# Kernel tuning notes

Measured on AMD Instinct MI355X. Metric: run time of the kernel, lower is better.

The kernel has to match this reference:

```python
import jax, jax.numpy as jnp
import numpy as np

LN_EPS = 1e-5
BN_EPS = 1e-5
ATTN_EPS = 1e-6

def _ln(x, g, b):
    m = x.mean(-1, keepdims=True)
    v = x.var(-1, keepdims=True)
    return (x - m) / jnp.sqrt(v + LN_EPS) * g + b

def setup_inputs() -> dict:
    key = jax.random.key(0)
    ks = jax.random.split(key, 16)
    B, C, N = 4, 256, 8192
    s = 0.05
    def rn(k, shape, scale=1.0):
        return jax.random.normal(k, shape, jnp.float32) * scale
    return {
        "x1": rn(ks[0], (B, C, N)),
        "x2": rn(ks[1], (B, C, N)),
        "Wq": rn(ks[2], (C, C), s), "bq": rn(ks[3], (C,), s),
        "Wk": rn(ks[4], (C, C), s), "bk": rn(ks[5], (C,), s),
        "Wv": rn(ks[6], (C, C), s), "bv": rn(ks[7], (C,), s),
        "threshold": jnp.array([0.1], jnp.float32),
        "W1": rn(ks[8], (2 * C, 2 * C), s),
        "W2": rn(ks[9], (C, 2 * C), s),
        "g1": jnp.ones((C,), jnp.float32), "b1": jnp.zeros((C,), jnp.float32),
        "g2": jnp.ones((C,), jnp.float32), "b2": jnp.zeros((C,), jnp.float32),
        "Wa": rn(ks[10], (C, C), s), "ba": rn(ks[11], (C,), s),
        "bn_g": jnp.ones((C,), jnp.float32), "bn_b": jnp.zeros((C,), jnp.float32),
        "bn_m": jnp.zeros((C,), jnp.float32), "bn_v": jnp.ones((C,), jnp.float32),
    }

def reference(x1, x2, Wq, bq, Wk, bk, Wv, bv, threshold, W1, W2,
              g1, b1, g2, b2, Wa, ba, bn_g, bn_b, bn_m, bn_v):
    B, C, N = x1.shape
    H = 4
    d = C // H
    def conv1x1(x, W, b):  # nn.Conv1d(C, C, 1): [B,C,N] -> [B,C,N]
        return jnp.einsum('bcn,oc->bon', x, W) + b[:, None]
    # projections -> [B, N, H, d]
    q = conv1x1(x1, Wq, bq).transpose(0, 2, 1).reshape(B, N, H, d)
    k = conv1x1(x2, Wk, bk).transpose(0, 2, 1).reshape(B, N, H, d)
    v = conv1x1(x2, Wv, bv).transpose(0, 2, 1).reshape(B, N, H, d)
    # DynamicSparseLinearAttention
    Q = jax.nn.elu(q) + 1.0
    K = jax.nn.elu(k) + 1.0
    S = v.shape[1]
    vals = v / S
    KV = jnp.einsum('nshd,nshv->nhdv', K, vals)               # [B,H,d,d]
    scores = jnp.einsum('nlhd,nhd->nlh', Q, K.sum(axis=1))    # [B,N,H]
    sparse = jnp.where(scores > threshold[0], scores, 0.0)
    Z = 1.0 / (sparse + ATTN_EPS)
    msg = jnp.einsum('nlhd,nhdv,nlh->nlhv', Q, KV, Z) * S     # [B,N,H,d]
    # view [B,N,C]; the transpose(1,2).transpose(1,2) in torch cancels
    msg = msg.reshape(B, N, H * d)
    msg = _ln(msg, g1, b1)
    msg = jnp.concatenate([x1.transpose(0, 2, 1), msg], axis=2)  # [B,N,2C]
    msg = jax.nn.relu(msg @ W1.T) @ W2.T                         # [B,N,C]
    msg = _ln(msg, g2, b2).transpose(0, 2, 1)                    # [B,C,N]
    # aug shortcut: conv1x1 + BatchNorm1d (eval mode, running stats)
    aug = conv1x1(x1, Wa, ba)
    aug = (aug - bn_m[None, :, None]) / jnp.sqrt(bn_v[None, :, None] + BN_EPS)
    aug = aug * bn_g[None, :, None] + bn_b[None, :, None]
    return msg + x1 + aug
```

## Files before the change

### kernel.cpp

```cpp
#include <hip/hip_runtime.h>

#define BB 4
#define CC 256
#define NN 8192
#define HH 4
#define NCH 16

typedef unsigned short u16;
typedef __bf16 bf16x8 __attribute__((ext_vector_type(8)));
typedef float f32x4 __attribute__((ext_vector_type(4)));

__device__ __forceinline__ float bf2f(unsigned u) {
  return __uint_as_float(u << 16);
}
__device__ __forceinline__ u16 f2bf(float f) {
  unsigned u = __float_as_uint(f);
  return (u16)((u + 0x7fffu + ((u >> 16) & 1u)) >> 16);
}
__device__ __forceinline__ void bf8_to_f32(uint4 r, float* f) {
  f[0] = __uint_as_float(r.x << 16); f[1] = __uint_as_float(r.x & 0xffff0000u);
  f[2] = __uint_as_float(r.y << 16); f[3] = __uint_as_float(r.y & 0xffff0000u);
  f[4] = __uint_as_float(r.z << 16); f[5] = __uint_as_float(r.z & 0xffff0000u);
  f[6] = __uint_as_float(r.w << 16); f[7] = __uint_as_float(r.w & 0xffff0000u);
}
__device__ __forceinline__ void bf4_to_f32(uint2 r, float* f) {
  f[0] = __uint_as_float(r.x << 16); f[1] = __uint_as_float(r.x & 0xffff0000u);
  f[2] = __uint_as_float(r.y << 16); f[3] = __uint_as_float(r.y & 0xffff0000u);
}
__device__ __forceinline__ void gload16(const u16* g, u16* l) {
  __builtin_amdgcn_global_load_lds(
      (const __attribute__((address_space(1))) unsigned int*)g,
      (__attribute__((address_space(3))) unsigned int*)l, 16, 0, 0);
}

__global__ __launch_bounds__(256) void cvt_all_kernel(
    const float* __restrict__ wq, const float* __restrict__ wk,
    const float* __restrict__ wv, const float* __restrict__ wa,
    const float* __restrict__ w1, const float* __restrict__ w2,
    u16* __restrict__ oq, u16* __restrict__ ok, u16* __restrict__ ov,
    u16* __restrict__ oa, u16* __restrict__ o1, u16* __restrict__ o2) {
  int i = blockIdx.x * 256 + threadIdx.x;
  const float* src;
  u16* dst;
  int off;
  if (i < 65536) { src = wq; dst = oq; off = i; }
  else if (i < 131072) { src = wk; dst = ok; off = i - 65536; }
  else if (i < 196608) { src = wv; dst = ov; off = i - 131072; }
  else if (i < 262144) { src = wa; dst = oa; off = i - 196608; }
  else if (i < 524288) { src = w1; dst = o1; off = i - 262144; }
  else { src = w2; dst = o2; off = i - 524288; }
  dst[off] = f2bf(src[off]);
}

__global__ __launch_bounds__(256) void transpose_kernel(const float* __restrict__ x1,
                                                        const float* __restrict__ x2,
                                                        u16* __restrict__ x1t,
                                                        u16* __restrict__ x2t) {
  __shared__ float T[64][65];
  const int bz = blockIdx.z;
  const int b = bz & 3;
  const float* x = (bz < 4) ? x1 : x2;
  u16* xt = (bz < 4) ? x1t : x2t;
  const int c0 = blockIdx.y * 64, n0 = blockIdx.x * 64;
  const float* xp = x + ((size_t)b * CC + c0) * NN + n0;
#pragma unroll
  for (int it = 0; it < 4; ++it) {
    int idx = threadIdx.x + it * 256;
    int r = idx >> 4, seg = idx & 15;
    float4 v = *(const float4*)(xp + (size_t)r * NN + seg * 4);
    T[r][seg * 4 + 0] = v.x; T[r][seg * 4 + 1] = v.y;
    T[r][seg * 4 + 2] = v.z; T[r][seg * 4 + 3] = v.w;
  }
  __syncthreads();
  u16* op = xt + ((size_t)b * NN + n0) * CC + c0;
  const int j = threadIdx.x >> 2, g = threadIdx.x & 3;
#pragma unroll
  for (int i = 0; i < 4; ++i) {
    int c = g * 16 + i * 4;
    uint2 pk;
    pk.x = (unsigned)f2bf(T[c + 0][j]) | ((unsigned)f2bf(T[c + 1][j]) << 16);
    pk.y = (unsigned)f2bf(T[c + 2][j]) | ((unsigned)f2bf(T[c + 3][j]) << 16);
    *(uint2*)(op + (size_t)j * CC + c) = pk;
  }
}

template <int MODE>
__global__ __launch_bounds__(256) void gemm_kernel(
    const u16* __restrict__ A1, const u16* __restrict__ A2,
    const u16* __restrict__ W, const float* __restrict__ bias,
    const float* __restrict__ e0, const float* __restrict__ e1,
    const float* __restrict__ e2, const float* __restrict__ e3,
    u16* __restrict__ outp, int K, int O) {
  __shared__ u16 As[128 * 64];
  __shared__ u16 Ws[128 * 64];
  const int m0 = blockIdx.x * 128, o0 = blockIdx.y * 128;
  const int tid = threadIdx.x, lane = tid & 63, wave = tid >> 6;
  const int wm = (wave >> 1) * 64, wo = (wave & 1) * 64;
  const int fr = lane & 15, fq = lane >> 4;
  f32x4 acc[4][4] = {};
  const int nkt = K >> 6;
  for (int kt = 0; kt < nkt; ++kt) {
    const int k0 = kt << 6;
    const u16* Ap;
    int rsA;
    if (MODE == 4) {
      Ap = (k0 < 256) ? (A1 + k0) : (A2 + (k0 - 256));
      rsA = 256;
    } else {
      Ap = A1 + k0;
      rsA = K;
    }
    const u16* Wp = W + k0;
#pragma unroll
    for (int i = 0; i < 4; ++i) {
      int idx = tid + i * 256;
      int rr = idx >> 3, ss = idx & 7;
      gload16(Ap + (size_t)(m0 + rr) * rsA + ss * 8, &As[(i * 256 + wave * 64) * 8]);
      gload16(Wp + (size_t)(o0 + rr) * K + ss * 8, &Ws[(i * 256 + wave * 64) * 8]);
    }
    __syncthreads();
#pragma unroll
    for (int kk = 0; kk < 2; ++kk) {
      bf16x8 af[4], bfr[4];
#pragma unroll
      for (int mi = 0; mi < 4; ++mi)
        af[mi] = __builtin_bit_cast(bf16x8, *(const uint4*)(&As[(wm + mi * 16 + fr) * 64 + kk * 32 + fq * 8]));
#pragma unroll
      for (int oi = 0; oi < 4; ++oi)
        bfr[oi] = __builtin_bit_cast(bf16x8, *(const uint4*)(&Ws[(wo + oi * 16 + fr) * 64 + kk * 32 + fq * 8]));
#pragma unroll
      for (int mi = 0; mi < 4; ++mi)
#pragma unroll
        for (int oi = 0; oi < 4; ++oi)
          acc[mi][oi] = __builtin_amdgcn_mfma_f32_16x16x32_bf16(af[mi], bfr[oi], acc[mi][oi], 0, 0, 0);
    }
    __syncthreads();
  }
  const int bb_ = m0 >> 13;
  const int nb = m0 & (NN - 1);
#pragma unroll
  for (int oi = 0; oi < 4; ++oi) {
    const int col = o0 + wo + oi * 16 + fr;
    float b0 = 0.f, sc = 1.f, sh = 0.f;
    if (MODE == 0 || MODE == 1 || MODE == 2) b0 = bias[col];
    if (MODE == 3) {
      sc = e0[col] * rsqrtf(e3[col] + 1e-5f);
      sh = (bias[col] - e2[col]) * sc + e1[col];
    }
#pragma unroll
    for (int mi = 0; mi < 4; ++mi) {
      const int rowb = m0 + wm + mi * 16 + fq * 4;
      if (MODE == 1 || MODE == 2) {
        float v[4];
#pragma unroll
        for (int r = 0; r < 4; ++r) {
          float t = acc[mi][oi][r] + b0;
          if (MODE == 1) t = (t > 0.f) ? (t + 1.f) : __expf(t);
          v[r] = t;
        }
        uint2 pk;
        pk.x = (unsigned)f2bf(v[0]) | ((unsigned)f2bf(v[1]) << 16);
        pk.y = (unsigned)f2bf(v[2]) | ((unsigned)f2bf(v[3]) << 16);
        const int nloc = nb + wm + mi * 16 + fq * 4;
        *(uint2*)(outp + ((size_t)bb_ * CC + col) * NN + nloc) = pk;
      } else {
#pragma unroll
        for (int r = 0; r < 4; ++r) {
          float v = acc[mi][oi][r];
          if (MODE == 0) {
            v += b0;
            v = (v > 0.f) ? (v + 1.f) : __expf(v);
          } else if (MODE == 3) {
            v = v * sc + sh;
          } else if (MODE == 4) {
            v = fmaxf(v, 0.f);
          }
          outp[(size_t)(rowb + r) * O + col] = f2bf(v);
        }
      }
    }
  }
}

__global__ __launch_bounds__(256) void ksum_kernel(const u16* __restrict__ K2,
                                                   float* __restrict__ Ksum) {
  __shared__ float red[4];
  const int b = blockIdx.y, c = blockIdx.x, tid = threadIdx.x;
  const u16* p = K2 + ((size_t)b * CC + c) * NN;
  float acc = 0.f;
#pragma unroll
  for (int j = 0; j < 4; ++j) {
    uint4 raw = *(const uint4*)(p + (j * 256 + tid) * 8);
    float f[8];
    bf8_to_f32(raw, f);
#pragma unroll
    for (int q = 0; q < 8; ++q) acc += f[q];
  }
#pragma unroll
  for (int m = 1; m < 64; m <<= 1) acc += __shfl_xor(acc, m);
  if ((tid & 63) == 0) red[tid >> 6] = acc;
  __syncthreads();
  if (tid == 0) Ksum[b * CC + c] = red[0] + red[1] + red[2] + red[3];
}

__global__ __launch_bounds__(256) void kvpartial_kernel(const u16* __restrict__ K2,
                                                        const u16* __restrict__ V2,
                                                        float* __restrict__ Pkv) {
  __shared__ u16 Ks[64 * 64];
  __shared__ u16 Vs[64 * 64];
  const int b = blockIdx.z, h = blockIdx.y, ch = blockIdx.x;
  const int tid = threadIdx.x, lane = tid & 63, w = tid >> 6;
  const int fr = lane & 15, fq = lane >> 4;
  const size_t base = ((size_t)b * CC + h * 64) * NN + (size_t)ch * (NN / NCH);
  f32x4 acc[4] = {};
  for (int step = 0; step < (NN / NCH) / 64; ++step) {
#pragma unroll
    for (int i = 0; i < 2; ++i) {
      int idx = tid + i * 256;
      int rr = idx >> 3, ss = idx & 7;
      gload16(K2 + base + (size_t)rr * NN + step * 64 + ss * 8, &Ks[(i * 256 + w * 64) * 8]);
      gload16(V2 + base + (size_t)rr * NN + step * 64 + ss * 8, &Vs[(i * 256 + w * 64) * 8]);
    }
    __syncthreads();
#pragma unroll
    for (int kk = 0; kk < 2; ++kk) {
      bf16x8 af = __builtin_bit_cast(bf16x8, *(const uint4*)(&Ks[(w * 16 + fr) * 64 + kk * 32 + fq * 8]));
#pragma unroll
      for (int oi = 0; oi < 4; ++oi) {
        bf16x8 bfr = __builtin_bit_cast(bf16x8, *(const uint4*)(&Vs[(oi * 16 + fr) * 64 + kk * 32 + fq * 8]));
        acc[oi] = __builtin_amdgcn_mfma_f32_16x16x32_bf16(af, bfr, acc[oi], 0, 0, 0);
      }
    }
    __syncthreads();
  }
  float* o = Pkv + (((size_t)ch * (BB * HH) + b * HH + h) << 12);
#pragma unroll
  for (int oi = 0; oi < 4; ++oi)
#pragma unroll
    for (int r = 0; r < 4; ++r)
      o[(w * 16 + fq * 4 + r) * 64 + oi * 16 + fr] = acc[oi][r];
}

__global__ __launch_bounds__(256) void kvreduce_kernel(const float* __restrict__ Pkv,
                                                       u16* __restrict__ KVT) {
  int i = blockIdx.x * 256 + threadIdx.x;
  int bh = i >> 12, dk = (i >> 6) & 63, dv = i & 63;
  float s = 0.f;
#pragma unroll
  for (int ch = 0; ch < NCH; ++ch)
    s += Pkv[(((size_t)ch * (BB * HH) + bh) << 12) + (dk << 6) + dv];
  KVT[((size_t)bh << 12) + (dv << 6) + dk] = f2bf(s);
}

__global__ __launch_bounds__(256) void msggemm_kernel(const u16* __restrict__ Qt,
                                                      const u16* __restrict__ KVT,
                                                      const float* __restrict__ Ksum,
                                                      const float* __restrict__ thrp,
                                                      u16* __restrict__ msgout) {
  __shared__ u16 As[128 * 64];
  __shared__ u16 Ws[64 * 64];
  __shared__ float Zs[128];
  const int m0 = blockIdx.x * 128, h = blockIdx.y, b = blockIdx.z;
  const int tid = threadIdx.x, lane = tid & 63, wave = tid >> 6;
  const int wm = (wave >> 1) * 64, wo = (wave & 1) * 32;
  const int fr = lane & 15, fq = lane >> 4;
  const float thrv = thrp[0];
  const u16* Ap = Qt + ((size_t)b * NN + m0) * CC + h * 64;
#pragma unroll
  for (int i = 0; i < 4; ++i) {
    int idx = tid + i * 256;
    int rr = idx >> 3, ss = idx & 7;
    gload16(Ap + (size_t)rr * CC + ss * 8, &As[(i * 256 + wave * 64) * 8]);
  }
  const u16* Wp = KVT + (((size_t)b * HH + h) << 12);
#pragma unroll
  for (int i = 0; i < 2; ++i) {
    int idx = tid + i * 256;
    int rr = idx >> 3, ss = idx & 7;
    gload16(Wp + (size_t)rr * 64 + ss * 8, &Ws[(i * 256 + wave * 64) * 8]);
  }
  __syncthreads();
  {
    const int row = tid >> 1, half = tid & 1;
    const float* ksh = Ksum + b * CC + h * 64 + half * 32;
    float za = 0.f;
#pragma unroll
    for (int j8 = 0; j8 < 4; ++j8) {
      uint4 raw = *(const uint4*)(&As[row * 64 + half * 32 + j8 * 8]);
      float f[8];
      bf8_to_f32(raw, f);
#pragma unroll
      for (int j = 0; j < 8; ++j) za += f[j] * ksh[j8 * 8 + j];
    }
    za += __shfl_xor(za, 1);
    if (half == 0) Zs[row] = 1.f / (((za > thrv) ? za : 0.f) + 1e-6f);
  }
  f32x4 acc[4][2] = {};
#pragma unroll
  for (int kk = 0; kk < 2; ++kk) {
    bf16x8 af[4], bfr[2];
#pragma unroll
    for (int mi = 0; mi < 4; ++mi)
      af[mi] = __builtin_bit_cast(bf16x8, *(const uint4*)(&As[(wm + mi * 16 + fr) * 64 + kk * 32 + fq * 8]));
#pragma unroll
    for (int oi = 0; oi < 2; ++oi)
      bfr[oi] = __builtin_bit_cast(bf16x8, *(const uint4*)(&Ws[(wo + oi * 16 + fr) * 64 + kk * 32 + fq * 8]));
#pragma unroll
    for (int mi = 0; mi < 4; ++mi)
#pragma unroll
      for (int oi = 0; oi < 2; ++oi)
        acc[mi][oi] = __builtin_amdgcn_mfma_f32_16x16x32_bf16(af[mi], bfr[oi], acc[mi][oi], 0, 0, 0);
  }
  __syncthreads();
#pragma unroll
  for (int oi = 0; oi < 2; ++oi) {
    const int col = h * 64 + wo + oi * 16 + fr;
#pragma unroll
    for (int mi = 0; mi < 4; ++mi) {
      const int rowb = wm + mi * 16 + fq * 4;
#pragma unroll
      for (int r = 0; r < 4; ++r) {
        const int row = rowb + r;
        msgout[((size_t)b * NN + m0 + row) * CC + col] = f2bf(acc[mi][oi][r] * Zs[row]);
      }
    }
  }
}

template <bool AUG>
__global__ __launch_bounds__(256) void ln_kernel(const u16* __restrict__ in,
                                                 u16* __restrict__ outb,
                                                 const float* __restrict__ g,
                                                 const float* __restrict__ bb,
                                                 const u16* __restrict__ aug) {
  const int tid = threadIdx.x, lane = tid & 63, w = tid >> 6;
  const size_t row0 = (size_t)blockIdx.x * 32;
  float gv[4], bv[4];
#pragma unroll
  for (int q = 0; q < 4; ++q) {
    gv[q] = g[lane * 4 + q];
    bv[q] = bb[lane * 4 + q];
  }
  for (int i = 0; i < 8; ++i) {
    const size_t row = row0 + i * 4 + w;
    uint2 raw = *(const uint2*)(in + row * CC + lane * 4);
    float v[4];
    bf4_to_f32(raw, v);
    float s1 = v[0] + v[1] + v[2] + v[3];
    float s2 = v[0] * v[0] + v[1] * v[1] + v[2] * v[2] + v[3] * v[3];
#pragma unroll
    for (int m = 1; m < 64; m <<= 1) {
      s1 += __shfl_xor(s1, m);
      s2 += __shfl_xor(s2, m);
    }
    const float mean = s1 * (1.f / CC);
    const float var = s2 * (1.f / CC) - mean * mean;
    const float rs = rsqrtf(var + 1e-5f);
    float ov[4];
#pragma unroll
    for (int q = 0; q < 4; ++q) ov[q] = (v[q] - mean) * rs * gv[q] + bv[q];
    if (AUG) {
      uint2 ar = *(const uint2*)(aug + row * CC + lane * 4);
      float af[4];
      bf4_to_f32(ar, af);
#pragma unroll
      for (int q = 0; q < 4; ++q) ov[q] += af[q];
    }
    uint2 pk;
    pk.x = (unsigned)f2bf(ov[0]) | ((unsigned)f2bf(ov[1]) << 16);
    pk.y = (unsigned)f2bf(ov[2]) | ((unsigned)f2bf(ov[3]) << 16);
    *(uint2*)(outb + row * CC + lane * 4) = pk;
  }
}

__global__ __launch_bounds__(256) void addout_kernel(const u16* __restrict__ tv,
                                                     const float* __restrict__ x1,
                                                     float* __restrict__ outp) {
  __shared__ float T[64][65];
  const int b = blockIdx.z, c0 = blockIdx.y * 64, n0 = blockIdx.x * 64;
  const u16* tp = tv + ((size_t)b * NN + n0) * CC + c0;
#pragma unroll
  for (int i = 0; i < 2; ++i) {
    int idx = threadIdx.x + i * 256;
    int r = idx >> 3, s = idx & 7;
    uint4 raw = *(const uint4*)(tp + (size_t)r * CC + s * 8);
    float f[8];
    bf8_to_f32(raw, f);
#pragma unroll
    for (int j = 0; j < 8; ++j) T[s * 8 + j][r] = f[j];
  }
  __syncthreads();
  const float* xp = x1 + ((size_t)b * CC + c0) * NN + n0;
  float* op = outp + ((size_t)b * CC + c0) * NN + n0;
#pragma unroll
  for (int i = 0; i < 16; ++i) {
    int idx = threadIdx.x + i * 256;
    int c = idx >> 6, j = idx & 63;
    op[(size_t)c * NN + j] = T[c][j] + xp[(size_t)c * NN + j];
  }
}

extern "C" void kernel_launch(void* const* d_in, const int* in_sizes, int n_in,
                              void* d_out, int out_size, void* d_ws, size_t ws_size,
                              hipStream_t stream) {
  (void)in_sizes; (void)n_in; (void)out_size; (void)ws_size;
  const float* x1 = (const float*)d_in[0];
  const float* x2 = (const float*)d_in[1];
  const float* Wq = (const float*)d_in[2];
  const float* bq = (const float*)d_in[3];
  const float* Wk = (const float*)d_in[4];
  const float* bk = (const float*)d_in[5];
  const float* Wv = (const float*)d_in[6];
  const float* bv = (const float*)d_in[7];
  const float* thr = (const float*)d_in[8];
  const float* W1 = (const float*)d_in[9];
  const float* W2 = (const float*)d_in[10];
  const float* g1 = (const float*)d_in[11];
  const float* b1 = (const float*)d_in[12];
  const float* g2 = (const float*)d_in[13];
  const float* b2 = (const float*)d_in[14];
  const float* Wa = (const float*)d_in[15];
  const float* ba = (const float*)d_in[16];
  const float* bng = (const float*)d_in[17];
  const float* bnb = (const float*)d_in[18];
  const float* bnm = (const float*)d_in[19];
  const float* bnv = (const float*)d_in[20];
  float* out = (float*)d_out;

  char* ws = (char*)d_ws;
  constexpr size_t SZ = (size_t)BB * NN * CC * sizeof(u16);
  u16* x1t = (u16*)(ws);
  u16* x2t = (u16*)(ws + SZ);
  u16* Qt = (u16*)(ws + 2 * SZ);
  u16* K2 = (u16*)(ws + 3 * SZ);
  u16* V2 = (u16*)(ws + 4 * SZ);
  u16* augt = (u16*)(ws + 5 * SZ);
  u16* msgout = (u16*)(ws + 6 * SZ);
  u16* h1 = Qt;
  u16* mlp2 = x2t;
  u16* msgN = V2;
  u16* tv = V2;
  float* Pkv = (float*)msgout;
  char* tail = ws + 7 * SZ;
  float* Ksum = (float*)tail;
  u16* KVT = (u16*)(tail + 4096);
  u16* Wqb = (u16*)(tail + 4096 + 131072);
  u16* Wkb = Wqb + CC * CC;
  u16* Wvb = Wkb + CC * CC;
  u16* Wab = Wvb + CC * CC;
  u16* W1b = Wab + CC * CC;
  u16* W2b = W1b + 512 * 512;

  cvt_all_kernel<<<dim3(2560), 256, 0, stream>>>(Wq, Wk, Wv, Wa, W1, W2,
                                                 Wqb, Wkb, Wvb, Wab, W1b, W2b);

  transpose_kernel<<<dim3(NN / 64, CC / 64, 2 * BB), 256, 0, stream>>>(x1, x2, x1t, x2t);

  gemm_kernel<0><<<dim3(256, 2), 256, 0, stream>>>(x1t, nullptr, Wqb, bq, nullptr, nullptr, nullptr, nullptr, Qt, 256, 256);
  gemm_kernel<1><<<dim3(256, 2), 256, 0, stream>>>(x2t, nullptr, Wkb, bk, nullptr, nullptr, nullptr, nullptr, K2, 256, 256);
  gemm_kernel<2><<<dim3(256, 2), 256, 0, stream>>>(x2t, nullptr, Wvb, bv, nullptr, nullptr, nullptr, nullptr, V2, 256, 256);
  gemm_kernel<3><<<dim3(256, 2), 256, 0, stream>>>(x1t, nullptr, Wab, ba, bng, bnb, bnm, bnv, augt, 256, 256);

  ksum_kernel<<<dim3(CC, BB), 256, 0, stream>>>(K2, Ksum);
  kvpartial_kernel<<<dim3(NCH, HH, BB), 256, 0, stream>>>(K2, V2, Pkv);
  kvreduce_kernel<<<dim3(256), 256, 0, stream>>>(Pkv, KVT);
  msggemm_kernel<<<dim3(NN / 128, HH, BB), 256, 0, stream>>>(Qt, KVT, Ksum, thr, msgout);
  ln_kernel<false><<<dim3(1024), 256, 0, stream>>>(msgout, msgN, g1, b1, nullptr);

  gemm_kernel<4><<<dim3(256, 4), 256, 0, stream>>>(x1t, msgN, W1b, nullptr, nullptr, nullptr, nullptr, nullptr, h1, 512, 512);
  gemm_kernel<5><<<dim3(256, 2), 256, 0, stream>>>(h1, nullptr, W2b, nullptr, nullptr, nullptr, nullptr, nullptr, mlp2, 512, 256);

  ln_kernel<true><<<dim3(1024), 256, 0, stream>>>(mlp2, tv, g2, b2, augt);
  addout_kernel<<<dim3(NN / 64, CC / 64, BB), 256, 0, stream>>>(tv, x1, out);
}
```

Baseline: 192.1 us.

## Fuse projections, Ksum, message LayerNorm, and MLP2 epilogue into fewer kernels

Merges the four projection GEMMs into one launch indexed by blockIdx.z. The K column sum is folded into the KV partial kernel and its reduction. The message GEMM now covers all heads per block and applies LayerNorm in LDS, and MLP2 is fused with the second LayerNorm, the aug add, the transpose back and the x1 residual. This cuts launches and intermediate global round trips. GEMM loads switch from global_load_lds to register-staged copies into padded LDS, which may change load efficiency and occupancy.

```diff
diff --git a/kernel.cpp b/kernel.cpp
--- a/kernel.cpp
+++ b/kernel.cpp
@@ -22,10 +22,6 @@
   f[2] = __uint_as_float(r.y << 16); f[3] = __uint_as_float(r.y & 0xffff0000u);
   f[4] = __uint_as_float(r.z << 16); f[5] = __uint_as_float(r.z & 0xffff0000u);
   f[6] = __uint_as_float(r.w << 16); f[7] = __uint_as_float(r.w & 0xffff0000u);
-}
-__device__ __forceinline__ void bf4_to_f32(uint2 r, float* f) {
-  f[0] = __uint_as_float(r.x << 16); f[1] = __uint_as_float(r.x & 0xffff0000u);
-  f[2] = __uint_as_float(r.y << 16); f[3] = __uint_as_float(r.y & 0xffff0000u);
 }
 __device__ __forceinline__ void gload16(const u16* g, u16* l) {
   __builtin_amdgcn_global_load_lds(
@@ -84,39 +80,36 @@
   }
 }
 
-template <int MODE>
-__global__ __launch_bounds__(256) void gemm_kernel(
-    const u16* __restrict__ A1, const u16* __restrict__ A2,
-    const u16* __restrict__ W, const float* __restrict__ bias,
-    const float* __restrict__ e0, const float* __restrict__ e1,
-    const float* __restrict__ e2, const float* __restrict__ e3,
-    u16* __restrict__ outp, int K, int O) {
-  __shared__ u16 As[128 * 64];
-  __shared__ u16 Ws[128 * 64];
+__global__ __launch_bounds__(256) void proj_all_kernel(
+    const u16* __restrict__ x1t, const u16* __restrict__ x2t,
+    const u16* __restrict__ Wqb, const u16* __restrict__ Wkb,
+    const u16* __restrict__ Wvb, const u16* __restrict__ Wab,
+    const float* __restrict__ bq, const float* __restrict__ bk,
+    const float* __restrict__ bv, const float* __restrict__ ba,
+    const float* __restrict__ bng, const float* __restrict__ bnb,
+    const float* __restrict__ bnm, const float* __restrict__ bnv,
+    u16* __restrict__ Qt, u16* __restrict__ K2, u16* __restrict__ V2,
+    u16* __restrict__ augt) {
+  __shared__ u16 As[128][72];
+  __shared__ u16 Ws[128][72];
+  const int mode = blockIdx.z;
+  const u16* A = (mode == 0 || mode == 3) ? x1t : x2t;
+  const u16* W = (mode == 0) ? Wqb : (mode == 1) ? Wkb : (mode == 2) ? Wvb : Wab;
+  const float* bias = (mode == 0) ? bq : (mode == 1) ? bk : (mode == 2) ? bv : ba;
+  u16* outp = (mode == 0) ? Qt : (mode == 1) ? K2 : (mode == 2) ? V2 : augt;
   const int m0 = blockIdx.x * 128, o0 = blockIdx.y * 128;
   const int tid = threadIdx.x, lane = tid & 63, wave = tid >> 6;
   const int wm = (wave >> 1) * 64, wo = (wave & 1) * 64;
   const int fr = lane & 15, fq = lane >> 4;
   f32x4 acc[4][4] = {};
-  const int nkt = K >> 6;
-  for (int kt = 0; kt < nkt; ++kt) {
+  for (int kt = 0; kt < 4; ++kt) {
     const int k0 = kt << 6;
-    const u16* Ap;
-    int rsA;
-    if (MODE == 4) {
-      Ap = (k0 < 256) ? (A1 + k0) : (A2 + (k0 - 256));
-      rsA = 256;
-    } else {
-      Ap = A1 + k0;
-      rsA = K;
-    }
-    const u16* Wp = W + k0;
 #pragma unroll
     for (int i = 0; i < 4; ++i) {
       int idx = tid + i * 256;
-      int rr = idx >> 3, ss = idx & 7;
-      gload16(Ap + (size_t)(m0 + rr) * rsA + ss * 8, &As[(i * 256 + wave * 64) * 8]);
-      gload16(Wp + (size_t)(o0 + rr) * K + ss * 8, &Ws[(i * 256 + wave * 64) * 8]);
+      int r = idx >> 3, s = idx & 7;
+      *(uint4*)(&As[r][s * 8]) = *(const uint4*)(A + (size_t)(m0 + r) * CC + k0 + s * 8);
+      *(uint4*)(&Ws[r][s * 8]) = *(const uint4*)(W + (size_t)(o0 + r) * CC + k0 + s * 8);
     }
     __syncthreads();
 #pragma unroll
@@ -124,10 +117,10 @@
       bf16x8 af[4], bfr[4];
 #pragma unroll
       for (int mi = 0; mi < 4; ++mi)
-        af[mi] = __builtin_bit_cast(bf16x8, *(const uint4*)(&As[(wm + mi * 16 + fr) * 64 + kk * 32 + fq * 8]));
+        af[mi] = __builtin_bit_cast(bf16x8, *(const uint4*)(&As[wm + mi * 16 + fr][kk * 32 + fq * 8]));
 #pragma unroll
       for (int oi = 0; oi < 4; ++oi)
-        bfr[oi] = __builtin_bit_cast(bf16x8, *(const uint4*)(&Ws[(wo + oi * 16 + fr) * 64 + kk * 32 + fq * 8]));
+        bfr[oi] = __builtin_bit_cast(bf16x8, *(const uint4*)(&Ws[wo + oi * 16 + fr][kk * 32 + fq * 8]));
 #pragma unroll
       for (int mi = 0; mi < 4; ++mi)
 #pragma unroll
@@ -141,21 +134,19 @@
 #pragma unroll
   for (int oi = 0; oi < 4; ++oi) {
     const int col = o0 + wo + oi * 16 + fr;
-    float b0 = 0.f, sc = 1.f, sh = 0.f;
-    if (MODE == 0 || MODE == 1 || MODE == 2) b0 = bias[col];
-    if (MODE == 3) {
-      sc = e0[col] * rsqrtf(e3[col] + 1e-5f);
-      sh = (bias[col] - e2[col]) * sc + e1[col];
+    float b0 = bias[col], sc = 1.f, sh = 0.f;
+    if (mode == 3) {
+      sc = bng[col] * rsqrtf(bnv[col] + 1e-5f);
+      sh = (b0 - bnm[col]) * sc + bnb[col];
     }
 #pragma unroll
     for (int mi = 0; mi < 4; ++mi) {
-      const int rowb = m0 + wm + mi * 16 + fq * 4;
-      if (MODE == 1 || MODE == 2) {
+      if (mode == 1 || mode == 2) {
         float v[4];
 #pragma unroll
         for (int r = 0; r < 4; ++r) {
           float t = acc[mi][oi][r] + b0;
-          if (MODE == 1) t = (t > 0.f) ? (t + 1.f) : __expf(t);
+          if (mode == 1) t = (t > 0.f) ? (t + 1.f) : __expf(t);
           v[r] = t;
         }
         uint2 pk;
@@ -164,48 +155,27 @@
         const int nloc = nb + wm + mi * 16 + fq * 4;
         *(uint2*)(outp + ((size_t)bb_ * CC + col) * NN + nloc) = pk;
       } else {
+        const int rowb = m0 + wm + mi * 16 + fq * 4;
 #pragma unroll
         for (int r = 0; r < 4; ++r) {
           float v = acc[mi][oi][r];
-          if (MODE == 0) {
+          if (mode == 0) {
             v += b0;
             v = (v > 0.f) ? (v + 1.f) : __expf(v);
-          } else if (MODE == 3) {
+          } else {
             v = v * sc + sh;
-          } else if (MODE == 4) {
-            v = fmaxf(v, 0.f);
           }
-          outp[(size_t)(rowb + r) * O + col] = f2bf(v);
+          outp[(size_t)(rowb + r) * CC + col] = f2bf(v);
         }
       }
     }
   }
-}
-
-__global__ __launch_bounds__(256) void ksum_kernel(const u16* __restrict__ K2,
-                                                   float* __restrict__ Ksum) {
-  __shared__ float red[4];
-  const int b = blockIdx.y, c = blockIdx.x, tid = threadIdx.x;
-  const u16* p = K2 + ((size_t)b * CC + c) * NN;
-  float acc = 0.f;
-#pragma unroll
-  for (int j = 0; j < 4; ++j) {
-    uint4 raw = *(const uint4*)(p + (j * 256 + tid) * 8);
-    float f[8];
-    bf8_to_f32(raw, f);
-#pragma unroll
-    for (int q = 0; q < 8; ++q) acc += f[q];
-  }
-#pragma unroll
-  for (int m = 1; m < 64; m <<= 1) acc += __shfl_xor(acc, m);
-  if ((tid & 63) == 0) red[tid >> 6] = acc;
-  __syncthreads();
-  if (tid == 0) Ksum[b * CC + c] = red[0] + red[1] + red[2] + red[3];
 }
 
 __global__ __launch_bounds__(256) void kvpartial_kernel(const u16* __restrict__ K2,
                                                         const u16* __restrict__ V2,
-                                                        float* __restrict__ Pkv) {
+                                                        float* __restrict__ Pkv,
+                                                        float* __restrict__ Pks) {
   __shared__ u16 Ks[64 * 64];
   __shared__ u16 Vs[64 * 64];
   const int b = blockIdx.z, h = blockIdx.y, ch = blockIdx.x;
@@ -213,6 +183,8 @@
   const int fr = lane & 15, fq = lane >> 4;
   const size_t base = ((size_t)b * CC + h * 64) * NN + (size_t)ch * (NN / NCH);
   f32x4 acc[4] = {};
+  const int krow = tid >> 2, kq = tid & 3;
+  float ksacc = 0.f;
   for (int step = 0; step < (NN / NCH) / 64; ++step) {
 #pragma unroll
     for (int i = 0; i < 2; ++i) {
@@ -223,6 +195,8 @@
     }
     __syncthreads();
 #pragma unroll
+    for (int j = 0; j < 16; ++j) ksacc += bf2f(Ks[krow * 64 + kq * 16 + j]);
+#pragma unroll
     for (int kk = 0; kk < 2; ++kk) {
       bf16x8 af = __builtin_bit_cast(bf16x8, *(const uint4*)(&Ks[(w * 16 + fr) * 64 + kk * 32 + fq * 8]));
 #pragma unroll
@@ -233,6 +207,9 @@
     }
     __syncthreads();
   }
+  ksacc += __shfl_xor(ksacc, 1);
+  ksacc += __shfl_xor(ksacc, 2);
+  if (kq == 0) Pks[((size_t)ch * BB + b) * CC + h * 64 + krow] = ksacc;
   float* o = Pkv + (((size_t)ch * (BB * HH) + b * HH + h) << 12);
 #pragma unroll
   for (int oi = 0; oi < 4; ++oi)
@@ -242,7 +219,9 @@
 }
 
 __global__ __launch_bounds__(256) void kvreduce_kernel(const float* __restrict__ Pkv,
-                                                       u16* __restrict__ KVT) {
+                                                       const float* __restrict__ Pks,
+                                                       u16* __restrict__ KVT,
+                                                       float* __restrict__ Ksum) {
   int i = blockIdx.x * 256 + threadIdx.x;
   int bh = i >> 12, dk = (i >> 6) & 63, dv = i & 63;
   float s = 0.f;
@@ -250,153 +229,289 @@
   for (int ch = 0; ch < NCH; ++ch)
     s += Pkv[(((size_t)ch * (BB * HH) + bh) << 12) + (dk << 6) + dv];
   KVT[((size_t)bh << 12) + (dv << 6) + dk] = f2bf(s);
-}
-
-__global__ __launch_bounds__(256) void msggemm_kernel(const u16* __restrict__ Qt,
-                                                      const u16* __restrict__ KVT,
-                                                      const float* __restrict__ Ksum,
-                                                      const float* __restrict__ thrp,
-                                                      u16* __restrict__ msgout) {
-  __shared__ u16 As[128 * 64];
-  __shared__ u16 Ws[64 * 64];
-  __shared__ float Zs[128];
-  const int m0 = blockIdx.x * 128, h = blockIdx.y, b = blockIdx.z;
-  const int tid = threadIdx.x, lane = tid & 63, wave = tid >> 6;
-  const int wm = (wave >> 1) * 64, wo = (wave & 1) * 32;
+  if (i < BB * CC) {
+    float t = 0.f;
+#pragma unroll
+    for (int ch = 0; ch < NCH; ++ch) t += Pks[ch * (BB * CC) + i];
+    Ksum[i] = t;
+  }
+}
+
+__global__ __launch_bounds__(256) void bigmsg_kernel(const u16* __restrict__ Qt,
+                                                     const u16* __restrict__ KVT,
+                                                     const float* __restrict__ Ksum,
+                                                     const float* __restrict__ thrp,
+                                                     const float* __restrict__ g1,
+                                                     const float* __restrict__ b1,
+                                                     u16* __restrict__ msgN) {
+  __shared__ u16 lds[64 * 264 + 4 * 64 * 72];
+  __shared__ float Zs[64 * 4];
+  u16* As = lds;
+  u16* Ws = lds + 64 * 264;
+  u16* Ml = lds;
+  const int m0 = blockIdx.x * 64;
+  const int b = blockIdx.z;
+  const int tid = threadIdx.x, lane = tid & 63, w = tid >> 6;
   const int fr = lane & 15, fq = lane >> 4;
-  const float thrv = thrp[0];
-  const u16* Ap = Qt + ((size_t)b * NN + m0) * CC + h * 64;
-#pragma unroll
-  for (int i = 0; i < 4; ++i) {
+  const u16* Ap = Qt + ((size_t)b * NN + m0) * CC;
+#pragma unroll
+  for (int i = 0; i < 8; ++i) {
     int idx = tid + i * 256;
-    int rr = idx >> 3, ss = idx & 7;
-    gload16(Ap + (size_t)rr * CC + ss * 8, &As[(i * 256 + wave * 64) * 8]);
-  }
-  const u16* Wp = KVT + (((size_t)b * HH + h) << 12);
-#pragma unroll
-  for (int i = 0; i < 2; ++i) {
+    int rr = idx >> 5, ss = idx & 31;
+    *(uint4*)(&As[rr * 264 + ss * 8]) = *(const uint4*)(Ap + (size_t)rr * CC + ss * 8);
+  }
+  const u16* Wp = KVT + ((size_t)(b * HH) << 12);
+#pragma unroll
+  for (int i = 0; i < 8; ++i) {
     int idx = tid + i * 256;
-    int rr = idx >> 3, ss = idx & 7;
-    gload16(Wp + (size_t)rr * 64 + ss * 8, &Ws[(i * 256 + wave * 64) * 8]);
+    int h = idx >> 9, rr = (idx >> 3) & 63, ss = idx & 7;
+    *(uint4*)(&Ws[(h * 64 + rr) * 72 + ss * 8]) = *(const uint4*)(Wp + ((size_t)h << 12) + rr * 64 + ss * 8);
   }
   __syncthreads();
   {
-    const int row = tid >> 1, half = tid & 1;
-    const float* ksh = Ksum + b * CC + h * 64 + half * 32;
+    const int row = tid >> 2, h = tid & 3;
+    const float* ks = Ksum + b * CC + h * 64;
     float za = 0.f;
 #pragma unroll
-    for (int j8 = 0; j8 < 4; ++j8) {
-      uint4 raw = *(const uint4*)(&As[row * 64 + half * 32 + j8 * 8]);
+    for (int j8 = 0; j8 < 8; ++j8) {
+      uint4 raw = *(const uint4*)(&As[row * 264 + h * 64 + j8 * 8]);
       float f[8];
       bf8_to_f32(raw, f);
 #pragma unroll
-      for (int j = 0; j < 8; ++j) za += f[j] * ksh[j8 * 8 + j];
-    }
-    za += __shfl_xor(za, 1);
-    if (half == 0) Zs[row] = 1.f / (((za > thrv) ? za : 0.f) + 1e-6f);
-  }
-  f32x4 acc[4][2] = {};
+      for (int j = 0; j < 8; ++j) za += f[j] * ks[j8 * 8 + j];
+    }
+    const float thrv = thrp[0];
+    Zs[row * 4 + h] = 1.f / (((za > thrv) ? za : 0.f) + 1e-6f);
+  }
+  f32x4 acc[4][4] = {};
 #pragma unroll
   for (int kk = 0; kk < 2; ++kk) {
-    bf16x8 af[4], bfr[2];
+    bf16x8 af[4], bfr[4];
 #pragma unroll
     for (int mi = 0; mi < 4; ++mi)
-      af[mi] = __builtin_bit_cast(bf16x8, *(const uint4*)(&As[(wm + mi * 16 + fr) * 64 + kk * 32 + fq * 8]));
-#pragma unroll
-    for (int oi = 0; oi < 2; ++oi)
-      bfr[oi] = __builtin_bit_cast(bf16x8, *(const uint4*)(&Ws[(wo + oi * 16 + fr) * 64 + kk * 32 + fq * 8]));
+      af[mi] = __builtin_bit_cast(bf16x8, *(const uint4*)(&As[(mi * 16 + fr) * 264 + w * 64 + kk * 32 + fq * 8]));
+#pragma unroll
+    for (int oi = 0; oi < 4; ++oi)
+      bfr[oi] = __builtin_bit_cast(bf16x8, *(const uint4*)(&Ws[(w * 64 + oi * 16 + fr) * 72 + kk * 32 + fq * 8]));
 #pragma unroll
     for (int mi = 0; mi < 4; ++mi)
 #pragma unroll
-      for (int oi = 0; oi < 2; ++oi)
+      for (int oi = 0; oi < 4; ++oi)
         acc[mi][oi] = __builtin_amdgcn_mfma_f32_16x16x32_bf16(af[mi], bfr[oi], acc[mi][oi], 0, 0, 0);
   }
   __syncthreads();
 #pragma unroll
-  for (int oi = 0; oi < 2; ++oi) {
-    const int col = h * 64 + wo + oi * 16 + fr;
+  for (int oi = 0; oi < 4; ++oi) {
+    const int col = w * 64 + oi * 16 + fr;
 #pragma unroll
     for (int mi = 0; mi < 4; ++mi) {
-      const int rowb = wm + mi * 16 + fq * 4;
 #pragma unroll
       for (int r = 0; r < 4; ++r) {
-        const int row = rowb + r;
-        msgout[((size_t)b * NN + m0 + row) * CC + col] = f2bf(acc[mi][oi][r] * Zs[row]);
-      }
-    }
-  }
-}
-
-template <bool AUG>
-__global__ __launch_bounds__(256) void ln_kernel(const u16* __restrict__ in,
-                                                 u16* __restrict__ outb,
-                                                 const float* __restrict__ g,
-                                                 const float* __restrict__ bb,
-                                                 const u16* __restrict__ aug) {
-  const int tid = threadIdx.x, lane = tid & 63, w = tid >> 6;
-  const size_t row0 = (size_t)blockIdx.x * 32;
-  float gv[4], bv[4];
-#pragma unroll
-  for (int q = 0; q < 4; ++q) {
-    gv[q] = g[lane * 4 + q];
-    bv[q] = bb[lane * 4 + q];
-  }
-  for (int i = 0; i < 8; ++i) {
-    const size_t row = row0 + i * 4 + w;
-    uint2 raw = *(const uint2*)(in + row * CC + lane * 4);
-    float v[4];
-    bf4_to_f32(raw, v);
-    float s1 = v[0] + v[1] + v[2] + v[3];
-    float s2 = v[0] * v[0] + v[1] * v[1] + v[2] * v[2] + v[3] * v[3];
-#pragma unroll
-    for (int m = 1; m < 64; m <<= 1) {
-      s1 += __shfl_xor(s1, m);
-      s2 += __shfl_xor(s2, m);
-    }
+        const int row = mi * 16 + fq * 4 + r;
+        Ml[row * 272 + col] = f2bf(acc[mi][oi][r] * Zs[row * 4 + w]);
+      }
+    }
+  }
+  __syncthreads();
+  {
+    const int row = tid >> 2, q = tid & 3;
+    const u16* mrow = &Ml[row * 272 + q * 64];
+    float s1 = 0.f, s2 = 0.f;
+#pragma unroll
+    for (int j8 = 0; j8 < 8; ++j8) {
+      uint4 raw = *(const uint4*)(mrow + j8 * 8);
+      float f[8];
+      bf8_to_f32(raw, f);
+#pragma unroll
+      for (int j = 0; j < 8; ++j) {
+        s1 += f[j];
+        s2 += f[j] * f[j];
+      }
+    }
+    s1 += __shfl_xor(s1, 1); s2 += __shfl_xor(s2, 1);
+    s1 += __shfl_xor(s1, 2); s2 += __shfl_xor(s2, 2);
     const float mean = s1 * (1.f / CC);
     const float var = s2 * (1.f / CC) - mean * mean;
     const float rs = rsqrtf(var + 1e-5f);
-    float ov[4];
-#pragma unroll
-    for (int q = 0; q < 4; ++q) ov[q] = (v[q] - mean) * rs * gv[q] + bv[q];
-    if (AUG) {
-      uint2 ar = *(const uint2*)(aug + row * CC + lane * 4);
-      float af[4];
-      bf4_to_f32(ar, af);
-#pragma unroll
-      for (int q = 0; q < 4; ++q) ov[q] += af[q];
-    }
-    uint2 pk;
-    pk.x = (unsigned)f2bf(ov[0]) | ((unsigned)f2bf(ov[1]) << 16);
-    pk.y = (unsigned)f2bf(ov[2]) | ((unsigned)f2bf(ov[3]) << 16);
-    *(uint2*)(outb + row * CC + lane * 4) = pk;
-  }
-}
-
-__global__ __launch_bounds__(256) void addout_kernel(const u16* __restrict__ tv,
-                                                     const float* __restrict__ x1,
-                                                     float* __restrict__ outp) {
-  __shared__ float T[64][65];
-  const int b = blockIdx.z, c0 = blockIdx.y * 64, n0 = blockIdx.x * 64;
-  const u16* tp = tv + ((size_t)b * NN + n0) * CC + c0;
-#pragma unroll
-  for (int i = 0; i < 2; ++i) {
-    int idx = threadIdx.x + i * 256;
-    int r = idx >> 3, s = idx & 7;
-    uint4 raw = *(const uint4*)(tp + (size_t)r * CC + s * 8);
-    float f[8];
-    bf8_to_f32(raw, f);
-#pragma unroll
-    for (int j = 0; j < 8; ++j) T[s * 8 + j][r] = f[j];
+    u16* orow = msgN + ((size_t)b * NN + m0 + row) * CC + q * 64;
+#pragma unroll
+    for (int j8 = 0; j8 < 8; ++j8) {
+      uint4 raw = *(const uint4*)(mrow + j8 * 8);
+      float f[8];
+      bf8_to_f32(raw, f);
+      const int cb = q * 64 + j8 * 8;
+      unsigned pk[4];
+#pragma unroll
+      for (int e = 0; e < 4; ++e) {
+        float lo = (f[2 * e] - mean) * rs * g1[cb + 2 * e] + b1[cb + 2 * e];
+        float hi = (f[2 * e + 1] - mean) * rs * g1[cb + 2 * e + 1] + b1[cb + 2 * e + 1];
+        pk[e] = (unsigned)f2bf(lo) | ((unsigned)f2bf(hi) << 16);
+      }
+      *(uint4*)(orow + j8 * 8) = make_uint4(pk[0], pk[1], pk[2], pk[3]);
+    }
+  }
+}
+
+__global__ __launch_bounds__(256) void mlp1_kernel(const u16* __restrict__ A1,
+                                                   const u16* __restrict__ A2,
+                                                   const u16* __restrict__ W,
+                                                   u16* __restrict__ outp) {
+  __shared__ u16 As[128][72];
+  __shared__ u16 Ws[128][72];
+  const int m0 = blockIdx.x * 128, o0 = blockIdx.y * 128;
+  const int tid = threadIdx.x, lane = tid & 63, wave = tid >> 6;
+  const int wm = (wave >> 1) * 64, wo = (wave & 1) * 64;
+  const int fr = lane & 15, fq = lane >> 4;
+  f32x4 acc[4][4] = {};
+  for (int kt = 0; kt < 8; ++kt) {
+    const int k0 = kt << 6;
+    const u16* Ap = (k0 < 256) ? (A1 + k0) : (A2 + (k0 - 256));
+#pragma unroll
+    for (int i = 0; i < 4; ++i) {
+      int idx = tid + i * 256;
+      int r = idx >> 3, s = idx & 7;
+      *(uint4*)(&As[r][s * 8]) = *(const uint4*)(Ap + (size_t)(m0 + r) * CC + s * 8);
+      *(uint4*)(&Ws[r][s * 8]) = *(const uint4*)(W + (size_t)(o0 + r) * 512 + k0 + s * 8);
+    }
+    __syncthreads();
+#pragma unroll
+    for (int kk = 0; kk < 2; ++kk) {
+      bf16x8 af[4], bfr[4];
+#pragma unroll
+      for (int mi = 0; mi < 4; ++mi)
+        af[mi] = __builtin_bit_cast(bf16x8, *(const uint4*)(&As[wm + mi * 16 + fr][kk * 32 + fq * 8]));
+#pragma unroll
+      for (int oi = 0; oi < 4; ++oi)
+        bfr[oi] = __builtin_bit_cast(bf16x8, *(const uint4*)(&Ws[wo + oi * 16 + fr][kk * 32 + fq * 8]));
+#pragma unroll
+      for (int mi = 0; mi < 4; ++mi)
+#pragma unroll
+        for (int oi = 0; oi < 4; ++oi)
+          acc[mi][oi] = __builtin_amdgcn_mfma_f32_16x16x32_bf16(af[mi], bfr[oi], acc[mi][oi], 0, 0, 0);
+    }
+    __syncthreads();
+  }
+#pragma unroll
+  for (int oi = 0; oi < 4; ++oi) {
+    const int col = o0 + wo + oi * 16 + fr;
+#pragma unroll
+    for (int mi = 0; mi < 4; ++mi) {
+      const int rowb = m0 + wm + mi * 16 + fq * 4;
+#pragma unroll
+      for (int r = 0; r < 4; ++r)
+        outp[(size_t)(rowb + r) * 512 + col] = f2bf(fmaxf(acc[mi][oi][r], 0.f));
+    }
+  }
+}
+
+__global__ __launch_bounds__(512) void mlp2fused_kernel(const u16* __restrict__ h1,
+                                                        const u16* __restrict__ W2b,
+                                                        const u16* __restrict__ augt,
+                                                        const float* __restrict__ x1,
+                                                        const float* __restrict__ g2,
+                                                        const float* __restrict__ b2,
+                                                        float* __restrict__ outp) {
+  __shared__ u16 lds[128 * 272];
+  u16* As = lds;
+  u16* Ws = lds + 128 * 72;
+  u16* Tl = lds;
+  const int m0 = blockIdx.x * 128;
+  const int b = m0 >> 13, nb = m0 & (NN - 1);
+  const int tid = threadIdx.x, lane = tid & 63, w = tid >> 6;
+  const int wm = (w >> 2) * 64, wo = (w & 3) * 64;
+  const int fr = lane & 15, fq = lane >> 4;
+  f32x4 acc[4][4] = {};
+  for (int kt = 0; kt < 8; ++kt) {
+    const int k0 = kt << 6;
+#pragma unroll
+    for (int i = 0; i < 2; ++i) {
+      int idx = tid + i * 512;
+      int rr = idx >> 3, ss = idx & 7;
+      *(uint4*)(&As[rr * 72 + ss * 8]) = *(const uint4*)(h1 + (size_t)(m0 + rr) * 512 + k0 + ss * 8);
+    }
+#pragma unroll
+    for (int i = 0; i < 4; ++i) {
+      int idx = tid + i * 512;
+      int rr = idx >> 3, ss = idx & 7;
+      *(uint4*)(&Ws[rr * 72 + ss * 8]) = *(const uint4*)(W2b + (size_t)rr * 512 + k0 + ss * 8);
+    }
+    __syncthreads();
+#pragma unroll
+    for (int kk = 0; kk < 2; ++kk) {
+      bf16x8 af[4], bfr[4];
+#pragma unroll
+      for (int mi = 0; mi < 4; ++mi)
+        af[mi] = __builtin_bit_cast(bf16x8, *(const uint4*)(&As[(wm + mi * 16 + fr) * 72 + kk * 32 + fq * 8]));
+#pragma unroll
+      for (int oi = 0; oi < 4; ++oi)
+        bfr[oi] = __builtin_bit_cast(bf16x8, *(const uint4*)(&Ws[(wo + oi * 16 + fr) * 72 + kk * 32 + fq * 8]));
+#pragma unroll
+      for (int mi = 0; mi < 4; ++mi)
+#pragma unroll
+        for (int oi = 0; oi < 4; ++oi)
+          acc[mi][oi] = __builtin_amdgcn_mfma_f32_16x16x32_bf16(af[mi], bfr[oi], acc[mi][oi], 0, 0, 0);
+    }
+    __syncthreads();
+  }
+#pragma unroll
+  for (int oi = 0; oi < 4; ++oi) {
+    const int col = wo + oi * 16 + fr;
+#pragma unroll
+    for (int mi = 0; mi < 4; ++mi) {
+#pragma unroll
+      for (int r = 0; r < 4; ++r) {
+        const int row = wm + mi * 16 + fq * 4 + r;
+        Tl[row * 272 + col] = f2bf(acc[mi][oi][r]);
+      }
+    }
   }
   __syncthreads();
-  const float* xp = x1 + ((size_t)b * CC + c0) * NN + n0;
-  float* op = outp + ((size_t)b * CC + c0) * NN + n0;
-#pragma unroll
-  for (int i = 0; i < 16; ++i) {
-    int idx = threadIdx.x + i * 256;
-    int c = idx >> 6, j = idx & 63;
-    op[(size_t)c * NN + j] = T[c][j] + xp[(size_t)c * NN + j];
+  {
+    const int row = tid >> 2, q = tid & 3;
+    u16* mrow = &Tl[row * 272 + q * 64];
+    float s1 = 0.f, s2 = 0.f;
+#pragma unroll
+    for (int j8 = 0; j8 < 8; ++j8) {
+      uint4 raw = *(const uint4*)(mrow + j8 * 8);
+      float f[8];
+      bf8_to_f32(raw, f);
+#pragma unroll
+      for (int j = 0; j < 8; ++j) {
+        s1 += f[j];
+        s2 += f[j] * f[j];
+      }
+    }
+    s1 += __shfl_xor(s1, 1); s2 += __shfl_xor(s2, 1);
+    s1 += __shfl_xor(s1, 2); s2 += __shfl_xor(s2, 2);
+    const float mean = s1 * (1.f / CC);
+    const float var = s2 * (1.f / CC) - mean * mean;
+    const float rs = rsqrtf(var + 1e-5f);
+    const u16* arow = augt + ((size_t)b * NN + nb + row) * CC + q * 64;
+#pragma unroll
+    for (int j8 = 0; j8 < 8; ++j8) {
+      uint4 raw = *(const uint4*)(mrow + j8 * 8);
+      uint4 ar = *(const uint4*)(arow + j8 * 8);
+      float f[8], af[8];
+      bf8_to_f32(raw, f);
+      bf8_to_f32(ar, af);
+      const int cb = q * 64 + j8 * 8;
+      unsigned pk[4];
+#pragma unroll
+      for (int e = 0; e < 4; ++e) {
+        float lo = (f[2 * e] - mean) * rs * g2[cb + 2 * e] + b2[cb + 2 * e] + af[2 * e];
+        float hi = (f[2 * e + 1] - mean) * rs * g2[cb + 2 * e + 1] + b2[cb + 2 * e + 1] + af[2 * e + 1];
+        pk[e] = (unsigned)f2bf(lo) | ((unsigned)f2bf(hi) << 16);
+      }
+      *(uint4*)(mrow + j8 * 8) = make_uint4(pk[0], pk[1], pk[2], pk[3]);
+    }
+  }
+  __syncthreads();
+#pragma unroll
+  for (int i = 0; i < 64; ++i) {
+    int idx = tid + i * 512;
+    int n = idx & 127, c = idx >> 7;
+    size_t off = ((size_t)b * CC + c) * NN + nb + n;
+    outp[off] = bf2f(Tl[n * 272 + c]) + x1[off];
   }
 }
 
@@ -435,16 +550,14 @@
   u16* K2 = (u16*)(ws + 3 * SZ);
   u16* V2 = (u16*)(ws + 4 * SZ);
   u16* augt = (u16*)(ws + 5 * SZ);
-  u16* msgout = (u16*)(ws + 6 * SZ);
+  float* Pkv = (float*)(ws + 6 * SZ);
   u16* h1 = Qt;
-  u16* mlp2 = x2t;
   u16* msgN = V2;
-  u16* tv = V2;
-  float* Pkv = (float*)msgout;
   char* tail = ws + 7 * SZ;
   float* Ksum = (float*)tail;
   u16* KVT = (u16*)(tail + 4096);
-  u16* Wqb = (u16*)(tail + 4096 + 131072);
+  float* Pks = (float*)(tail + 4096 + 131072);
+  u16* Wqb = (u16*)(tail + 4096 + 131072 + 65536);
   u16* Wkb = Wqb + CC * CC;
   u16* Wvb = Wkb + CC * CC;
   u16* Wab = Wvb + CC * CC;
@@ -453,23 +566,13 @@
 
   cvt_all_kernel<<<dim3(2560), 256, 0, stream>>>(Wq, Wk, Wv, Wa, W1, W2,
                                                  Wqb, Wkb, Wvb, Wab, W1b, W2b);
-
   transpose_kernel<<<dim3(NN / 64, CC / 64, 2 * BB), 256, 0, stream>>>(x1, x2, x1t, x2t);
-
-  gemm_kernel<0><<<dim3(256, 2), 256, 0, stream>>>(x1t, nullptr, Wqb, bq, nullptr, nullptr, nullptr, nullptr, Qt, 256, 256);
-  gemm_kernel<1><<<dim3(256, 2), 256, 0, stream>>>(x2t, nullptr, Wkb, bk, nullptr, nullptr, nullptr, nullptr, K2, 256, 256);
-  gemm_kernel<2><<<dim3(256, 2), 256, 0, stream>>>(x2t, nullptr, Wvb, bv, nullptr, nullptr, nullptr, nullptr, V2, 256, 256);
-  gemm_kernel<3><<<dim3(256, 2), 256, 0, stream>>>(x1t, nullptr, Wab, ba, bng, bnb, bnm, bnv, augt, 256, 256);
-
-  ksum_kernel<<<dim3(CC, BB), 256, 0, stream>>>(K2, Ksum);
-  kvpartial_kernel<<<dim3(NCH, HH, BB), 256, 0, stream>>>(K2, V2, Pkv);
-  kvreduce_kernel<<<dim3(256), 256, 0, stream>>>(Pkv, KVT);
-  msggemm_kernel<<<dim3(NN / 128, HH, BB), 256, 0, stream>>>(Qt, KVT, Ksum, thr, msgout);
-  ln_kernel<false><<<dim3(1024), 256, 0, stream>>>(msgout, msgN, g1, b1, nullptr);
-
-  gemm_kernel<4><<<dim3(256, 4), 256, 0, stream>>>(x1t, msgN, W1b, nullptr, nullptr, nullptr, nullptr, nullptr, h1, 512, 512);
-  gemm_kernel<5><<<dim3(256, 2), 256, 0, stream>>>(h1, nullptr, W2b, nullptr, nullptr, nullptr, nullptr, nullptr, mlp2, 512, 256);
-
-  ln_kernel<true><<<dim3(1024), 256, 0, stream>>>(mlp2, tv, g2, b2, augt);
-  addout_kernel<<<dim3(NN / 64, CC / 64, BB), 256, 0, stream>>>(tv, x1, out);
-}
+  proj_all_kernel<<<dim3(256, 2, 4), 256, 0, stream>>>(
+      x1t, x2t, Wqb, Wkb, Wvb, Wab, bq, bk, bv, ba, bng, bnb, bnm, bnv,
+      Qt, K2, V2, augt);
+  kvpartial_kernel<<<dim3(NCH, HH, BB), 256, 0, stream>>>(K2, V2, Pkv, Pks);
+  kvreduce_kernel<<<dim3(256), 256, 0, stream>>>(Pkv, Pks, KVT, Ksum);
+  bigmsg_kernel<<<dim3(NN / 64, 1, BB), 256, 0, stream>>>(Qt, KVT, Ksum, thr, g1, b1, msgN);
+  mlp1_kernel<<<dim3(256, 4), 256, 0, stream>>>(x1t, msgN, W1b, h1);
+  mlp2fused_kernel<<<dim3(256), 512, 0, stream>>>(h1, W2b, augt, x1, g2, b2, out);
+}
```

Result: faster. 184.9 us (-3.7%).
